# Kernel optimization log

Hardware: AMD Instinct MI355X
Metric: run time of the kernel (lower is better)

## Reference

```python
import jax, jax.numpy as jnp
import numpy as np

# TT config: input_dimension=2048, output_multiplier=4, rank=16
# top_ranks    = [8,2,2,2,2,2,2,2,2]  (prod = 2048)
# bottom_ranks = [8,2,2,2,2,2,2,2,2]  (prod = 2048)
# core shapes (top, bottom, left, right): left/right are TT bond ranks.
CORE_SHAPES = [(8, 8, 1, 16)] + [(2, 2, 16, 16)] * 7 + [(2, 2, 16, 1)]


def setup_inputs() -> dict:
    key = jax.random.key(0)
    ks = jax.random.split(key, 10)
    inp = {"x": jax.random.normal(ks[0], (4, 2048, 2048), dtype=jnp.float32)}
    for i, s in enumerate(CORE_SHAPES):
        inp[f"p{i}"] = jax.random.normal(ks[i + 1], s, dtype=jnp.float32)
    return inp


def _tt_apply(x, ps):
    # x: [B, S, D] with D = prod(top_ranks) = 2048
    B, S, D = x.shape
    T = B * S
    # Normalize every core to (top, bottom, left_bond_in, right_bond_out).
    # Original einsum: '... abcdefghi, ajs, bkst, cltu, dmuv, envw, fowx, gpxy, hqzy, irz -> ... jklmnopqr'
    # Core 7 ('hqzy') has swapped bonds: its 4th dim (y) is the incoming bond
    # from core 6 and its 3rd dim (z) is the outgoing bond into core 8 ('irz').
    cores = list(ps[:7]) + [jnp.transpose(ps[7], (0, 1, 3, 2)), ps[8]]
    # core 0 is used as p0[:, :, 0, :] in the original; its left dim is 1 so
    # keeping the singleton left axis is identical math.
    y = x.reshape(T, 1, 1, D)  # [T, out_so_far=1, bond=1, remaining_top=D]
    J, M = 1, D
    for g in cores:
        tk, bk, lk, rk = g.shape
        y = y.reshape(T, J, lk, tk, M // tk)
        # contract incoming bond l and current top index a with the core
        y = jnp.einsum('tjlam,ablr->tjbrm', y, g)
        J *= bk
        M //= tk
        y = y.reshape(T, J, rk, M)
    # final: rk == 1, M == 1 -> [T, J] with J = prod(bottom_ranks) = 2048
    return y.reshape(B, S, J)


def reference(x, p0, p1, p2, p3, p4, p5, p6, p7, p8):
    return _tt_apply(x, (p0, p1, p2, p3, p4, p5, p6, p7, p8))
```

## Files before the change

kernel.cpp:

```cpp
#include <hip/hip_runtime.h>
#include <stdint.h>

typedef unsigned short u16;
typedef __bf16 bf16x8 __attribute__((ext_vector_type(8)));
typedef float f32x16 __attribute__((ext_vector_type(16)));
typedef u16 u16x8 __attribute__((ext_vector_type(8)));

__device__ __forceinline__ u16 f2bf(float f) {
  uint32_t u = __float_as_uint(f);
  u += 0x7fffu + ((u >> 16) & 1u);
  return (u16)(u >> 16);
}

__global__ __launch_bounds__(256) void build_lr_kernel(
    const float* __restrict__ p0, const float* __restrict__ p1,
    const float* __restrict__ p2, const float* __restrict__ p3,
    const float* __restrict__ p4, const float* __restrict__ p5,
    const float* __restrict__ p6, const float* __restrict__ p7,
    const float* __restrict__ p8, float* __restrict__ L4, float* __restrict__ R) {
  __shared__ float sA[16384];
  __shared__ float sB[4096];
  const int tid = threadIdx.x;
  if (blockIdx.x < 16) {
    for (int i = tid; i < 1024; i += 256) sA[i] = p0[i];
    __syncthreads();
    for (int i = tid; i < 4096; i += 256) {
      int r = i & 15, t = i >> 4;
      int Bb = t & 15, Aa = t >> 4;
      int a = Aa & 1, A = Aa >> 1, b = Bb & 1, B = Bb >> 1;
      const float* srow = sA + (A * 8 + B) * 16;
      const float* g = p1 + ((a * 2 + b) * 16) * 16 + r;
      float s = 0.f;
#pragma unroll
      for (int l = 0; l < 16; l++) s += srow[l] * g[l * 16];
      sB[i] = s;
    }
    __syncthreads();
    for (int i = tid; i < 16384; i += 256) {
      int r = i & 15, t = i >> 4;
      int Bb = t & 31, Aa = t >> 5;
      int a = Aa & 1, A = Aa >> 1, b = Bb & 1, B = Bb >> 1;
      const float* srow = sB + (A * 16 + B) * 16;
      const float* g = p2 + ((a * 2 + b) * 16) * 16 + r;
      float s = 0.f;
#pragma unroll
      for (int l = 0; l < 16; l++) s += srow[l] * g[l * 16];
      sA[i] = s;
    }
    __syncthreads();
    int gi = blockIdx.x * 256 + tid;
    int b3 = gi & 1, a3 = (gi >> 1) & 1;
    int B2 = (gi >> 2) & 31, A2 = gi >> 7;
    const float* srow = sA + (A2 * 32 + B2) * 16;
    const float* g3 = p3 + ((a3 * 2 + b3) * 16) * 16;
    float tmp[16];
#pragma unroll
    for (int r3 = 0; r3 < 16; r3++) {
      float s = 0.f;
#pragma unroll
      for (int r2 = 0; r2 < 16; r2++) s += srow[r2] * g3[r2 * 16 + r3];
      tmp[r3] = s;
    }
#pragma unroll
    for (int ab = 0; ab < 4; ab++) {
      int a4 = ab >> 1, b4 = ab & 1;
      const float* g4 = p4 + (ab * 16) * 16;
      int AL = A2 * 4 + a3 * 2 + a4;
      int BL = B2 * 4 + b3 * 2 + b4;
      float* drow = L4 + (AL * 128 + BL) * 16;
#pragma unroll
      for (int r4 = 0; r4 < 16; r4++) {
        float s = 0.f;
#pragma unroll
        for (int r3 = 0; r3 < 16; r3++) s += tmp[r3] * g4[r3 * 16 + r4];
        drow[r4] = s;
      }
    }
  } else {
    for (int i = tid; i < 64; i += 256) sA[i] = p8[i];
    __syncthreads();
    for (int i = tid; i < 256; i += 256) {
      int rl = i & 15, t = i >> 4;
      int Bt = t & 3, At = t >> 2;
      int a = At >> 1, Ap = At & 1, b = Bt >> 1, Bp = Bt & 1;
      const float* srow = sA + (Ap * 2 + Bp) * 16;
      const float* g = p7 + ((a * 2 + b) * 16) * 16 + rl;
      float s = 0.f;
#pragma unroll
      for (int rk = 0; rk < 16; rk++) s += srow[rk] * g[rk * 16];
      sB[i] = s;
    }
    __syncthreads();
    for (int i = tid; i < 1024; i += 256) {
      int rl = i & 15, t = i >> 4;
      int Bt = t & 7, At = t >> 3;
      int a = At >> 2, Ap = At & 3, b = Bt >> 2, Bp = Bt & 3;
      const float* srow = sB + (Ap * 4 + Bp) * 16;
      const float* g = p6 + (((a * 2 + b) * 16) + rl) * 16;
      float s = 0.f;
#pragma unroll
      for (int rk = 0; rk < 16; rk++) s += srow[rk] * g[rk];
      sA[i] = s;
    }
    __syncthreads();
    for (int i = tid; i < 4096; i += 256) {
      int rl = i & 15, t = i >> 4;
      int Bt = t & 15, At = t >> 4;
      int a = At >> 3, Ap = At & 7, b = Bt >> 3, Bp = Bt & 7;
      const float* srow = sA + (Ap * 8 + Bp) * 16;
      const float* g = p5 + (((a * 2 + b) * 16) + rl) * 16;
      float s = 0.f;
#pragma unroll
      for (int rk = 0; rk < 16; rk++) s += srow[rk] * g[rk];
      R[i] = s;
    }
  }
}

__global__ __launch_bounds__(256) void merge_kernel(const float* __restrict__ L4,
                                                    const float* __restrict__ R,
                                                    u16* __restrict__ Wt) {
  int t = blockIdx.x * 256 + threadIdx.x;
  int e = t * 8;
  int Af = e & 2047;
  int Bf = e >> 11;
  const float* lrow = L4 + ((Af >> 4) * 128 + (Bf >> 4)) * 16;
  float lv[16];
#pragma unroll
  for (int r = 0; r < 16; r++) lv[r] = lrow[r];
  const float* rbase = R + (Bf & 15) * 16;
  u16x8 o;
#pragma unroll
  for (int j = 0; j < 8; j++) {
    const float* rrow = rbase + ((Af + j) & 15) * 256;
    float s = 0.f;
#pragma unroll
    for (int r = 0; r < 16; r++) s += lv[r] * rrow[r];
    o[j] = f2bf(s);
  }
  *(u16x8*)(Wt + (size_t)Bf * 2048 + Af) = o;
}

__global__ __launch_bounds__(256) void cast_x_kernel(const float* __restrict__ x,
                                                     u16* __restrict__ xb) {
  size_t i = ((size_t)blockIdx.x * 256 + threadIdx.x) * 8;
  float4 u = *(const float4*)(x + i);
  float4 v = *(const float4*)(x + i + 4);
  u16x8 o;
  o[0] = f2bf(u.x); o[1] = f2bf(u.y); o[2] = f2bf(u.z); o[3] = f2bf(u.w);
  o[4] = f2bf(v.x); o[5] = f2bf(v.y); o[6] = f2bf(v.z); o[7] = f2bf(v.w);
  *(u16x8*)(xb + i) = o;
}

__global__ __launch_bounds__(256, 2) void gemm_kernel(const u16* __restrict__ A,
                                                      const u16* __restrict__ B,
                                                      float* __restrict__ C) {
  __shared__ u16 As[256 * 32];
  __shared__ u16 Bs[128 * 32];
  const int tid = threadIdx.x;
  const int lane = tid & 63;
  const int w = tid >> 6;
  const int m0 = blockIdx.y * 256;
  const int n0 = blockIdx.x * 128;
  const int wm = w * 64;
  const int r32 = lane & 31;
  const int half = lane >> 5;
  const int lrow = lane >> 2;
  const int oct = (lane & 3) ^ ((lrow >> 1) & 3);

  const u16* gaA = A + (size_t)(m0 + w * 16 + lrow) * 2048 + oct * 8;
  const u16* gaB = B + (size_t)(n0 + w * 16 + lrow) * 2048 + oct * 8;

  const int sw = (r32 >> 1) & 3;

  f32x16 acc[2][4] = {};

  for (int k0 = 0; k0 < 2048; k0 += 32) {
#pragma unroll
    for (int q = 0; q < 4; q++)
      __builtin_amdgcn_global_load_lds(
          (const __attribute__((address_space(1))) void*)(gaA + k0 + (size_t)q * 64 * 2048),
          (__attribute__((address_space(3))) void*)(As + (q * 4 + w) * 512), 16, 0, 0);
#pragma unroll
    for (int q = 0; q < 2; q++)
      __builtin_amdgcn_global_load_lds(
          (const __attribute__((address_space(1))) void*)(gaB + k0 + (size_t)q * 64 * 2048),
          (__attribute__((address_space(3))) void*)(Bs + (q * 4 + w) * 512), 16, 0, 0);
    __syncthreads();
    bf16x8 af[2][2], bv[4][2];
#pragma unroll
    for (int mt = 0; mt < 2; mt++)
#pragma unroll
      for (int ks = 0; ks < 2; ks++)
        af[mt][ks] = *(const bf16x8*)(As + (wm + mt * 32 + r32) * 32 +
                                      ((ks * 2 + half) ^ sw) * 8);
#pragma unroll
    for (int nt = 0; nt < 4; nt++)
#pragma unroll
      for (int ks = 0; ks < 2; ks++)
        bv[nt][ks] = *(const bf16x8*)(Bs + (nt * 32 + r32) * 32 +
                                      ((ks * 2 + half) ^ sw) * 8);
#pragma unroll
    for (int ks = 0; ks < 2; ks++)
#pragma unroll
      for (int mt = 0; mt < 2; mt++)
#pragma unroll
        for (int nt = 0; nt < 4; nt++)
          acc[mt][nt] = __builtin_amdgcn_mfma_f32_32x32x16_bf16(af[mt][ks], bv[nt][ks], acc[mt][nt], 0, 0, 0);
    __syncthreads();
  }
#pragma unroll
  for (int mt = 0; mt < 2; mt++) {
#pragma unroll
    for (int nt = 0; nt < 4; nt++) {
      size_t cbase = (size_t)(m0 + wm + mt * 32 + 4 * half) * 2048 + (n0 + nt * 32 + r32);
#pragma unroll
      for (int reg = 0; reg < 16; reg++) {
        int row = (reg & 3) + 8 * (reg >> 2);
        __builtin_nontemporal_store(acc[mt][nt][reg], C + cbase + (size_t)row * 2048);
      }
    }
  }
}

extern "C" void kernel_launch(void* const* d_in, const int* in_sizes, int n_in,
                              void* d_out, int out_size, void* d_ws, size_t ws_size,
                              hipStream_t stream) {
  const float* x = (const float*)d_in[0];
  const float* p0 = (const float*)d_in[1];
  const float* p1 = (const float*)d_in[2];
  const float* p2 = (const float*)d_in[3];
  const float* p3 = (const float*)d_in[4];
  const float* p4 = (const float*)d_in[5];
  const float* p5 = (const float*)d_in[6];
  const float* p6 = (const float*)d_in[7];
  const float* p7 = (const float*)d_in[8];
  const float* p8 = (const float*)d_in[9];
  char* ws = (char*)d_ws;
  u16* xbf = (u16*)ws;
  u16* Wt = (u16*)(ws + 33554432);
  float* L4 = (float*)(ws + 41943040);
  float* R = (float*)(ws + 42991616);

  build_lr_kernel<<<17, 256, 0, stream>>>(p0, p1, p2, p3, p4, p5, p6, p7, p8, L4, R);
  merge_kernel<<<2048, 256, 0, stream>>>(L4, R, Wt);
  cast_x_kernel<<<8192, 256, 0, stream>>>(x, xbf);
  gemm_kernel<<<dim3(16, 32), 256, 0, stream>>>(xbf, Wt, (float*)d_out);
}
```

Measured before the change: 270.5 us.

## Rewrite GEMM as 256x256 tile, 8-wave, double-buffered K=64 pipeline; merge prep kernels

Replaces the 256x128 single-stage GEMM with a 512-thread, 256x256-tile kernel. It double-buffers K=64 slices in LDS and interleaves global-to-LDS loads with MFMA phases, using explicit barriers, sched_barriers, setprio and partial vmcnt waits. Blocks are remapped for better L2 locality, and the merge and cast kernels are fused into one launch. The goal is to hide memory latency behind MFMA work and raise arithmetic intensity, at the cost of much larger LDS use and more registers, which may limit occupancy.

```diff
diff --git a/kernel.cpp b/kernel.cpp
--- a/kernel.cpp
+++ b/kernel.cpp
@@ -117,110 +117,188 @@
   }
 }
 
-__global__ __launch_bounds__(256) void merge_kernel(const float* __restrict__ L4,
-                                                    const float* __restrict__ R,
-                                                    u16* __restrict__ Wt) {
-  int t = blockIdx.x * 256 + threadIdx.x;
-  int e = t * 8;
-  int Af = e & 2047;
-  int Bf = e >> 11;
-  const float* lrow = L4 + ((Af >> 4) * 128 + (Bf >> 4)) * 16;
-  float lv[16];
-#pragma unroll
-  for (int r = 0; r < 16; r++) lv[r] = lrow[r];
-  const float* rbase = R + (Bf & 15) * 16;
-  u16x8 o;
-#pragma unroll
-  for (int j = 0; j < 8; j++) {
-    const float* rrow = rbase + ((Af + j) & 15) * 256;
-    float s = 0.f;
-#pragma unroll
-    for (int r = 0; r < 16; r++) s += lv[r] * rrow[r];
-    o[j] = f2bf(s);
+__global__ __launch_bounds__(256) void prep_kernel(const float* __restrict__ L4,
+                                                   const float* __restrict__ R,
+                                                   u16* __restrict__ Wt,
+                                                   const float* __restrict__ x,
+                                                   u16* __restrict__ xb) {
+  if (blockIdx.x < 2048) {
+    int t = blockIdx.x * 256 + threadIdx.x;
+    int e = t * 8;
+    int Af = e & 2047;
+    int Bf = e >> 11;
+    const float* lrow = L4 + ((Af >> 4) * 128 + (Bf >> 4)) * 16;
+    float lv[16];
+#pragma unroll
+    for (int r = 0; r < 16; r++) lv[r] = lrow[r];
+    const float* rbase = R + (Bf & 15) * 16;
+    u16x8 o;
+#pragma unroll
+    for (int j = 0; j < 8; j++) {
+      const float* rrow = rbase + ((Af + j) & 15) * 256;
+      float s = 0.f;
+#pragma unroll
+      for (int r = 0; r < 16; r++) s += lv[r] * rrow[r];
+      o[j] = f2bf(s);
+    }
+    *(u16x8*)(Wt + (size_t)Bf * 2048 + Af) = o;
+  } else {
+    size_t i = ((size_t)(blockIdx.x - 2048) * 256 + threadIdx.x) * 8;
+    float4 u = *(const float4*)(x + i);
+    float4 v = *(const float4*)(x + i + 4);
+    u16x8 o;
+    o[0] = f2bf(u.x); o[1] = f2bf(u.y); o[2] = f2bf(u.z); o[3] = f2bf(u.w);
+    o[4] = f2bf(v.x); o[5] = f2bf(v.y); o[6] = f2bf(v.z); o[7] = f2bf(v.w);
+    *(u16x8*)(xb + i) = o;
   }
-  *(u16x8*)(Wt + (size_t)Bf * 2048 + Af) = o;
-}
-
-__global__ __launch_bounds__(256) void cast_x_kernel(const float* __restrict__ x,
-                                                     u16* __restrict__ xb) {
-  size_t i = ((size_t)blockIdx.x * 256 + threadIdx.x) * 8;
-  float4 u = *(const float4*)(x + i);
-  float4 v = *(const float4*)(x + i + 4);
-  u16x8 o;
-  o[0] = f2bf(u.x); o[1] = f2bf(u.y); o[2] = f2bf(u.z); o[3] = f2bf(u.w);
-  o[4] = f2bf(v.x); o[5] = f2bf(v.y); o[6] = f2bf(v.z); o[7] = f2bf(v.w);
-  *(u16x8*)(xb + i) = o;
-}
-
-__global__ __launch_bounds__(256, 2) void gemm_kernel(const u16* __restrict__ A,
+}
+
+#define SB0() __builtin_amdgcn_sched_barrier(0)
+
+#define STAGE_OP(g, S, h, dsto, gk)                                            \
+  __builtin_amdgcn_global_load_lds(                                            \
+      (const __attribute__((address_space(1))) void*)(g[h][0] + (gk)),         \
+      (__attribute__((address_space(3))) void*)(S + (dsto) + ldst), 16, 0, 0); \
+  __builtin_amdgcn_global_load_lds(                                            \
+      (const __attribute__((address_space(1))) void*)(g[h][1] + (gk)),         \
+      (__attribute__((address_space(3))) void*)(S + (dsto) + ldst + 4096), 16, 0, 0);
+
+#define STAGE_A(h, dsto, gk) STAGE_OP(gA, As, h, dsto, gk)
+#define STAGE_B(h, dsto, gk) STAGE_OP(gB, Bs, h, dsto, gk)
+
+#define LOAD_AF(ah, pa)                                                        \
+  _Pragma("unroll") for (int m = 0; m < 2; m++)                                \
+      _Pragma("unroll") for (int ks = 0; ks < 4; ks++)                         \
+          af[m][ks] = *(const bf16x8*)(As + (pa) + (ah) * 8192 + rbA +         \
+                                       m * 2048 + ((((ks * 2) + hl) ^ key) * 8));
+
+#define LOAD_BV(bh, pa)                                                        \
+  _Pragma("unroll") for (int ks = 0; ks < 4; ks++)                             \
+      bv[ks] = *(const bf16x8*)(Bs + (pa) + (bh) * 8192 + rbB +                \
+                                ((((ks * 2) + hl) ^ key) * 8));
+
+#define MFMA8(ah, bh)                                                          \
+  _Pragma("unroll") for (int ks = 0; ks < 4; ks++) {                           \
+    acc[ah][bh][0] = __builtin_amdgcn_mfma_f32_32x32x16_bf16(                  \
+        af[0][ks], bv[ks], acc[ah][bh][0], 0, 0, 0);                           \
+    acc[ah][bh][1] = __builtin_amdgcn_mfma_f32_32x32x16_bf16(                  \
+        af[1][ks], bv[ks], acc[ah][bh][1], 0, 0, 0);                           \
+  }
+
+#define PH_MID()                                                               \
+  SB0();                                                                       \
+  asm volatile("s_barrier" ::: "memory");                                      \
+  asm volatile("s_waitcnt lgkmcnt(0)" ::: "memory");                           \
+  SB0();                                                                       \
+  __builtin_amdgcn_s_setprio(1);
+
+#define PH_END()                                                               \
+  __builtin_amdgcn_s_setprio(0);                                               \
+  SB0();                                                                       \
+  asm volatile("s_barrier" ::: "memory");                                      \
+  SB0();
+
+#define PH_END_VM()                                                            \
+  __builtin_amdgcn_s_setprio(0);                                               \
+  SB0();                                                                       \
+  asm volatile("s_waitcnt vmcnt(6)" ::: "memory");                             \
+  asm volatile("s_barrier" ::: "memory");                                      \
+  SB0();
+
+__global__ __launch_bounds__(512, 2) void gemm_kernel(const u16* __restrict__ A,
                                                       const u16* __restrict__ B,
                                                       float* __restrict__ C) {
-  __shared__ u16 As[256 * 32];
-  __shared__ u16 Bs[128 * 32];
+  __shared__ alignas(128) u16 As[4 * 8192];
+  __shared__ alignas(128) u16 Bs[4 * 8192];
   const int tid = threadIdx.x;
   const int lane = tid & 63;
   const int w = tid >> 6;
-  const int m0 = blockIdx.y * 256;
-  const int n0 = blockIdx.x * 128;
-  const int wm = w * 64;
+  const int wr = w >> 2;
+  const int wc = w & 3;
   const int r32 = lane & 31;
-  const int half = lane >> 5;
-  const int lrow = lane >> 2;
-  const int oct = (lane & 3) ^ ((lrow >> 1) & 3);
-
-  const u16* gaA = A + (size_t)(m0 + w * 16 + lrow) * 2048 + oct * 8;
-  const u16* gaB = B + (size_t)(n0 + w * 16 + lrow) * 2048 + oct * 8;
-
-  const int sw = (r32 >> 1) & 3;
-
-  f32x16 acc[2][4] = {};
-
-  for (int k0 = 0; k0 < 2048; k0 += 32) {
-#pragma unroll
-    for (int q = 0; q < 4; q++)
-      __builtin_amdgcn_global_load_lds(
-          (const __attribute__((address_space(1))) void*)(gaA + k0 + (size_t)q * 64 * 2048),
-          (__attribute__((address_space(3))) void*)(As + (q * 4 + w) * 512), 16, 0, 0);
-#pragma unroll
-    for (int q = 0; q < 2; q++)
-      __builtin_amdgcn_global_load_lds(
-          (const __attribute__((address_space(1))) void*)(gaB + k0 + (size_t)q * 64 * 2048),
-          (__attribute__((address_space(3))) void*)(Bs + (q * 4 + w) * 512), 16, 0, 0);
-    __syncthreads();
-    bf16x8 af[2][2], bv[4][2];
-#pragma unroll
-    for (int mt = 0; mt < 2; mt++)
-#pragma unroll
-      for (int ks = 0; ks < 2; ks++)
-        af[mt][ks] = *(const bf16x8*)(As + (wm + mt * 32 + r32) * 32 +
-                                      ((ks * 2 + half) ^ sw) * 8);
-#pragma unroll
-    for (int nt = 0; nt < 4; nt++)
-#pragma unroll
-      for (int ks = 0; ks < 2; ks++)
-        bv[nt][ks] = *(const bf16x8*)(Bs + (nt * 32 + r32) * 32 +
-                                      ((ks * 2 + half) ^ sw) * 8);
-#pragma unroll
-    for (int ks = 0; ks < 2; ks++)
-#pragma unroll
-      for (int mt = 0; mt < 2; mt++)
-#pragma unroll
-        for (int nt = 0; nt < 4; nt++)
-          acc[mt][nt] = __builtin_amdgcn_mfma_f32_32x32x16_bf16(af[mt][ks], bv[nt][ks], acc[mt][nt], 0, 0, 0);
-    __syncthreads();
+  const int hl = lane >> 5;
+
+  const int F = blockIdx.x + (blockIdx.y << 3);
+  const int li = F >> 3;
+  const int m0 = ((F & 7) * 4 + (li >> 3)) << 8;
+  const int n0 = (li & 7) << 8;
+
+  const int srow = lane >> 3;
+  const int soct = (lane & 7) ^ srow;
+  const u16* gA[2][2];
+  const u16* gB[2][2];
+#pragma unroll
+  for (int h = 0; h < 2; h++)
+#pragma unroll
+    for (int q = 0; q < 2; q++) {
+      int r = h * 128 + q * 64 + w * 8 + srow;
+      gA[h][q] = A + (size_t)(m0 + r) * 2048 + soct * 8;
+      gB[h][q] = B + (size_t)(n0 + r) * 2048 + soct * 8;
+    }
+  const int ldst = w * 512;
+
+  const int key = r32 & 7;
+  const int rbA = (wr * 64 + r32) * 64;
+  const int rbB = (wc * 32 + r32) * 64;
+
+  f32x16 acc[2][2][2] = {};
+  bf16x8 af[2][4], bv[4];
+
+  STAGE_A(0, 0, 0);      SB0();
+  STAGE_B(1, 8192, 0);   SB0();
+  STAGE_A(1, 8192, 0);   SB0();
+  STAGE_B(0, 0, 0);      SB0();
+  STAGE_A(0, 16384, 64); SB0();
+  STAGE_B(1, 24576, 64); SB0();
+  STAGE_A(1, 24576, 64); SB0();
+  asm volatile("s_waitcnt vmcnt(6)" ::: "memory");
+  asm volatile("s_barrier" ::: "memory");
+  SB0();
+
+  for (int t = 0; t < 32; t++) {
+    const int pa = (t & 1) << 14;
+    const int pan = 16384 - pa;
+    const int k1 = (t + 1 < 32 ? t + 1 : 31) * 64;
+    const int k2 = (t + 2 < 32 ? t + 2 : 31) * 64;
+    LOAD_AF(0, pa);
+    LOAD_BV(0, pa);
+    STAGE_B(0, pan, k1);
+    PH_MID();
+    MFMA8(0, 0);
+    PH_END();
+    LOAD_BV(1, pa);
+    STAGE_A(0, pa, k2);
+    PH_MID();
+    MFMA8(0, 1);
+    PH_END();
+    LOAD_AF(1, pa);
+    STAGE_B(1, pa + 8192, k2);
+    PH_MID();
+    MFMA8(1, 1);
+    PH_END();
+    LOAD_BV(0, pa);
+    STAGE_A(1, pa + 8192, k2);
+    PH_MID();
+    MFMA8(1, 0);
+    PH_END_VM();
   }
-#pragma unroll
-  for (int mt = 0; mt < 2; mt++) {
-#pragma unroll
-    for (int nt = 0; nt < 4; nt++) {
-      size_t cbase = (size_t)(m0 + wm + mt * 32 + 4 * half) * 2048 + (n0 + nt * 32 + r32);
-#pragma unroll
-      for (int reg = 0; reg < 16; reg++) {
-        int row = (reg & 3) + 8 * (reg >> 2);
-        __builtin_nontemporal_store(acc[mt][nt][reg], C + cbase + (size_t)row * 2048);
+
+  asm volatile("s_waitcnt vmcnt(0)" ::: "memory");
+
+#pragma unroll
+  for (int ah = 0; ah < 2; ah++)
+#pragma unroll
+    for (int bh = 0; bh < 2; bh++)
+#pragma unroll
+      for (int m = 0; m < 2; m++) {
+        size_t cbase = (size_t)(m0 + ah * 128 + wr * 64 + m * 32 + 4 * hl) * 2048 +
+                       (n0 + bh * 128 + wc * 32 + r32);
+#pragma unroll
+        for (int reg = 0; reg < 16; reg++) {
+          int row = (reg & 3) + 8 * (reg >> 2);
+          __builtin_nontemporal_store(acc[ah][bh][m][reg], C + cbase + (size_t)row * 2048);
+        }
       }
-    }
-  }
 }
 
 extern "C" void kernel_launch(void* const* d_in, const int* in_sizes, int n_in,
@@ -243,7 +321,6 @@
   float* R = (float*)(ws + 42991616);
 
   build_lr_kernel<<<17, 256, 0, stream>>>(p0, p1, p2, p3, p4, p5, p6, p7, p8, L4, R);
-  merge_kernel<<<2048, 256, 0, stream>>>(L4, R, Wt);
-  cast_x_kernel<<<8192, 256, 0, stream>>>(x, xbf);
-  gemm_kernel<<<dim3(16, 32), 256, 0, stream>>>(xbf, Wt, (float*)d_out);
-}
+  prep_kernel<<<10240, 256, 0, stream>>>(L4, R, Wt, x, xbf);
+  gemm_kernel<<<dim3(8, 32), 512, 0, stream>>>(xbf, Wt, (float*)d_out);
+}
```

Result: no change. 271.0 us (+0.2%).
